# Kernel tuning notes

Hardware: AMD Instinct MI355X
Metric: run time of the kernel (lower is better)

The kernel has to match this reference:

```python
import jax, jax.numpy as jnp
import numpy as np

N_NODES = 50000
N_EDGES = 800000
N_FEAT = 128
N_GRAPHS = 512
OUT_DIM = 128


def gcn_conv(x, W, b, src, dst, ew, n):
    """PyG GCNConv: h = x @ W; add self-loops (weight 1); symmetric norm
    D^-1/2 A D^-1/2 with edge weights; scatter-add messages src->dst; + bias."""
    h = x @ W  # [n, out]
    loop = jnp.arange(n)
    s = jnp.concatenate([src, loop])
    d = jnp.concatenate([dst, loop])
    w = jnp.concatenate([ew, jnp.ones((n,), x.dtype)])
    deg = jax.ops.segment_sum(w, d, num_segments=n)
    dinv = jnp.where(deg > 0, jax.lax.rsqrt(deg), 0.0)
    norm = dinv[s] * w * dinv[d]  # [E+n]
    out = jax.ops.segment_sum(h[s] * norm[:, None], d, num_segments=n)
    return out + b


def setup_inputs() -> dict:
    key = jax.random.key(0)
    ks = jax.random.split(key, 12)
    F = N_FEAT
    x = jax.random.normal(ks[0], (N_NODES, F), jnp.float32)
    edge_index = jax.random.randint(ks[1], (2, N_EDGES), 0, N_NODES, jnp.int64)
    edge_attr = jax.random.uniform(ks[2], (N_EDGES,), jnp.float32)
    # deterministic sorted graph assignment -> no empty graphs (avoids -inf in max pool)
    batch = (jnp.arange(N_NODES, dtype=jnp.int64) * N_GRAPHS) // N_NODES
    def lin(k, fi, fo):
        s = 1.0 / np.sqrt(fi)
        return jax.random.uniform(k, (fi, fo), jnp.float32, -s, s)
    return {
        "x": x, "edge_attr": edge_attr,
        "W1": lin(ks[3], F, F), "b1": jnp.zeros((F,), jnp.float32),
        "W2": lin(ks[4], F, 2 * F), "b2": jnp.zeros((2 * F,), jnp.float32),
        "W3": lin(ks[5], 2 * F, 4 * F), "b3": jnp.zeros((4 * F,), jnp.float32),
        "Wf1": lin(ks[6], 4 * F, 1024), "bf1": jnp.zeros((1024,), jnp.float32),
        "Wf2": lin(ks[7], 1024, OUT_DIM), "bf2": jnp.zeros((OUT_DIM,), jnp.float32),
        "edge_index": edge_index, "batch": batch,
    }


def reference(x, edge_attr, W1, b1, W2, b2, W3, b3, Wf1, bf1, Wf2, bf2,
              edge_index, batch):
    n = x.shape[0]
    src, dst = edge_index[0], edge_index[1]
    h = jax.nn.relu(gcn_conv(x, W1, b1, src, dst, edge_attr, n))
    h = jax.nn.relu(gcn_conv(h, W2, b2, src, dst, edge_attr, n))
    h = jax.nn.relu(gcn_conv(h, W3, b3, src, dst, edge_attr, n))
    # global max pool over nodes per graph
    g = jax.ops.segment_max(h, batch, num_segments=N_GRAPHS)  # [G, 4F]
    g = jax.nn.relu(g @ Wf1 + bf1)
    # dropout is identity in eval mode
    out = g @ Wf2 + bf2
    return out
```

## Files before the change

kernel.cpp:

```cpp
#include <hip/hip_runtime.h>

#define NNODES 50000
#define NEDGES 800000
#define NGRAPH 512
#define DCAP 64

typedef short bf16x8 __attribute__((ext_vector_type(8)));
typedef unsigned short u16x8 __attribute__((ext_vector_type(8)));
typedef float f32x4 __attribute__((ext_vector_type(4)));
typedef unsigned long long u64;

static __device__ __forceinline__ float b2f(unsigned short u) {
    return __uint_as_float(((unsigned)u) << 16);
}
static __device__ __forceinline__ unsigned short f2b(float f) {
    unsigned u = __float_as_uint(f);
    unsigned r = (u + 0x7fffu + ((u >> 16) & 1u)) >> 16;
    return (unsigned short)r;
}

static __device__ __forceinline__ void ldrow(const unsigned short* X, size_t off, float (&v)[2]) {
    unsigned u = *(const unsigned*)(X + off);
    v[0] = b2f((unsigned short)(u & 0xffff));
    v[1] = b2f((unsigned short)(u >> 16));
}
static __device__ __forceinline__ void ldrow(const unsigned short* X, size_t off, float (&v)[4]) {
    uint2 u = *(const uint2*)(X + off);
    v[0] = b2f((unsigned short)(u.x & 0xffff));
    v[1] = b2f((unsigned short)(u.x >> 16));
    v[2] = b2f((unsigned short)(u.y & 0xffff));
    v[3] = b2f((unsigned short)(u.y >> 16));
}

__global__ void k_setup(u64* deg_cnt, int* gp) {
    int i = blockIdx.x * 256 + threadIdx.x;
    if (i < NNODES) deg_cnt[i] = (u64)(1u << 24);
    if (i < NGRAPH * 512) gp[i] = 0;
}

__global__ __launch_bounds__(256) void k_count(const int4* __restrict__ ei_s,
                                               const int4* __restrict__ ei_d,
                                               const float4* __restrict__ ew4,
                                               u64* deg_cnt,
                                               unsigned* __restrict__ edges) {
    int t = blockIdx.x * 256 + threadIdx.x;
    if (t >= NEDGES / 4) return;
    int4 ss = ei_s[t];
    int4 dd = ei_d[t];
    float4 ww = ew4[t];
    int s[4] = {ss.x, ss.y, ss.z, ss.w};
    int d[4] = {dd.x, dd.y, dd.z, dd.w};
    float w[4] = {ww.x, ww.y, ww.z, ww.w};
    int slot[4];
    #pragma unroll
    for (int u = 0; u < 4; ++u) {
        unsigned fixed = __float2uint_rn(w[u] * 16777216.0f);
        u64 old = atomicAdd(&deg_cnt[d[u]], ((u64)1 << 32) | fixed);
        slot[u] = (int)(old >> 32);
        if (slot[u] > DCAP - 1) slot[u] = DCAP - 1;
    }
    #pragma unroll
    for (int u = 0; u < 4; ++u)
        edges[((unsigned)d[u] << 6) | slot[u]] = ((unsigned)f2b(w[u]) << 16) | (unsigned)s[u];
}

__global__ void k_prep(const u64* __restrict__ deg_cnt, float* __restrict__ dinv) {
    int i = blockIdx.x * 256 + threadIdx.x;
    if (i < NNODES)
        dinv[i] = rsqrtf((float)(unsigned)(deg_cnt[i] & 0xffffffffull) * 5.9604645e-8f);
}

__global__ void k_wt_all(const float* __restrict__ W1, const float* __restrict__ W2,
                         const float* __restrict__ W3, const float* __restrict__ Wf1,
                         const float* __restrict__ Wf2,
                         unsigned short* __restrict__ T1, unsigned short* __restrict__ T2,
                         unsigned short* __restrict__ T3, unsigned short* __restrict__ Tf1,
                         unsigned short* __restrict__ Tf2) {
    int i = blockIdx.x * 256 + threadIdx.x;
    const float* W; unsigned short* T; int K, ns;
    if (i < 16384)        { W = W1;  T = T1;  K = 128;  ns = 7;  }
    else if (i < 49152)   { W = W2;  T = T2;  K = 128;  ns = 8;  i -= 16384; }
    else if (i < 180224)  { W = W3;  T = T3;  K = 256;  ns = 9;  i -= 49152; }
    else if (i < 704512)  { W = Wf1; T = Tf1; K = 512;  ns = 10; i -= 180224; }
    else if (i < 835584)  { W = Wf2; T = Tf2; K = 1024; ns = 7;  i -= 704512; }
    else return;
    int k = i >> ns, n = i & ((1 << ns) - 1);
    T[(size_t)n * K + k] = f2b(W[i]);
}

__global__ void k_cvt4(const float* __restrict__ X, const float* __restrict__ dinv,
                       unsigned short* __restrict__ Y, int n4) {
    int i = blockIdx.x * 256 + threadIdx.x;
    if (i < n4) {
        float4 v = ((const float4*)X)[i];
        float d = dinv[i >> 5];
        uint2 o;
        o.x = (unsigned)f2b(v.x * d) | ((unsigned)f2b(v.y * d) << 16);
        o.y = (unsigned)f2b(v.z * d) | ((unsigned)f2b(v.w * d) << 16);
        ((uint2*)Y)[i] = o;
    }
}

template <int VEC>
__global__ __launch_bounds__(256) void k_aggregate(const unsigned short* __restrict__ X,
                                                   const u64* __restrict__ deg_cnt,
                                                   const unsigned* __restrict__ edges,
                                                   const float* __restrict__ dinv,
                                                   unsigned short* __restrict__ Z) {
    const int F = 64 * VEC;
    const int wave = threadIdx.x >> 6, lane = threadIdx.x & 63;
    const int node = blockIdx.x * 4 + wave;
    if (node >= NNODES) return;
    const int fo = lane * VEC;
    const float di = dinv[node];
    const int cnt = (int)(deg_cnt[node] >> 32);
    const unsigned* erow = edges + ((unsigned)node << 6);

    float acc[VEC], v[VEC];
    ldrow(X, (size_t)node * F + fo, v);
    #pragma unroll
    for (int j = 0; j < VEC; ++j) acc[j] = v[j];

    int e = 0;
    for (; e + 8 <= cnt; e += 8) {
        unsigned pk[8];
        float vv[8][VEC];
        #pragma unroll
        for (int u = 0; u < 8; ++u) pk[u] = erow[e + u];
        #pragma unroll
        for (int u = 0; u < 8; ++u) ldrow(X, (size_t)(pk[u] & 0xffffu) * F + fo, vv[u]);
        #pragma unroll
        for (int u = 0; u < 8; ++u) {
            float c = b2f((unsigned short)(pk[u] >> 16));
            #pragma unroll
            for (int j = 0; j < VEC; ++j) acc[j] += c * vv[u][j];
        }
    }
    for (; e + 4 <= cnt; e += 4) {
        unsigned pk[4];
        float vv[4][VEC];
        #pragma unroll
        for (int u = 0; u < 4; ++u) pk[u] = erow[e + u];
        #pragma unroll
        for (int u = 0; u < 4; ++u) ldrow(X, (size_t)(pk[u] & 0xffffu) * F + fo, vv[u]);
        #pragma unroll
        for (int u = 0; u < 4; ++u) {
            float c = b2f((unsigned short)(pk[u] >> 16));
            #pragma unroll
            for (int j = 0; j < VEC; ++j) acc[j] += c * vv[u][j];
        }
    }
    for (; e < cnt; ++e) {
        unsigned pe = erow[e];
        float c = b2f((unsigned short)(pe >> 16));
        ldrow(X, (size_t)(pe & 0xffffu) * F + fo, v);
        #pragma unroll
        for (int j = 0; j < VEC; ++j) acc[j] += c * v[j];
    }

    if constexpr (VEC == 2) {
        unsigned o = (unsigned)f2b(di * acc[0]) | ((unsigned)f2b(di * acc[1]) << 16);
        *(unsigned*)(Z + (size_t)node * F + fo) = o;
    } else {
        uint2 o;
        o.x = (unsigned)f2b(di * acc[0]) | ((unsigned)f2b(di * acc[1]) << 16);
        o.y = (unsigned)f2b(di * acc[2]) | ((unsigned)f2b(di * acc[3]) << 16);
        *(uint2*)(Z + (size_t)node * F + fo) = o;
    }
}

template <int CMODE, int AFP>
__global__ __launch_bounds__(256) void k_gemm_mfma(const void* __restrict__ Av,
                                                   const unsigned short* __restrict__ WT,
                                                   const float* __restrict__ bias,
                                                   void* __restrict__ Cv,
                                                   const int* __restrict__ batch,
                                                   int* __restrict__ gp,
                                                   const float* __restrict__ rscale,
                                                   int M, int N, int K) {
    constexpr int LDK = 40;
    __shared__ unsigned short As[64 * LDK];
    __shared__ unsigned short Bs[128 * LDK];
    const int tid = threadIdx.x;
    const int m0 = blockIdx.y * 64, n0 = blockIdx.x * 128;
    const int wave = tid >> 6, lane = tid & 63;
    const int wm = (wave >> 1) * 32;
    const int wn = (wave & 1) * 64;
    const int quad = lane >> 4, mrow = lane & 15;

    const int ar = tid >> 2;
    const int ak = (tid & 3) * 8;
    const bool arow_ok = (m0 + ar) < M;
    const size_t aoff = (size_t)(m0 + ar) * K + ak;
    const unsigned short* Bg0 = WT + (size_t)(n0 + ar) * K + ak;
    const unsigned short* Bg1 = WT + (size_t)(n0 + ar + 64) * K + ak;

    f32x4 acc[2][4] = {};

    for (int k0 = 0; k0 < K; k0 += 32) {
        u16x8 av = {};
        if (arow_ok) {
            if constexpr (AFP) {
                const float* Af = (const float*)Av + aoff + k0;
                float4 f0 = *(const float4*)Af;
                float4 f1 = *(const float4*)(Af + 4);
                av[0] = (short)f2b(f0.x); av[1] = (short)f2b(f0.y);
                av[2] = (short)f2b(f0.z); av[3] = (short)f2b(f0.w);
                av[4] = (short)f2b(f1.x); av[5] = (short)f2b(f1.y);
                av[6] = (short)f2b(f1.z); av[7] = (short)f2b(f1.w);
            } else {
                av = *(const u16x8*)((const unsigned short*)Av + aoff + k0);
            }
        }
        u16x8 bv0 = *(const u16x8*)(Bg0 + k0);
        u16x8 bv1 = *(const u16x8*)(Bg1 + k0);
        *(u16x8*)&As[ar * LDK + ak] = av;
        *(u16x8*)&Bs[ar * LDK + ak] = bv0;
        *(u16x8*)&Bs[(ar + 64) * LDK + ak] = bv1;
        __syncthreads();
        bf16x8 af[2], bf[4];
        #pragma unroll
        for (int mt = 0; mt < 2; ++mt)
            af[mt] = *(const bf16x8*)&As[(wm + mt * 16 + mrow) * LDK + quad * 8];
        #pragma unroll
        for (int nt = 0; nt < 4; ++nt)
            bf[nt] = *(const bf16x8*)&Bs[(wn + nt * 16 + mrow) * LDK + quad * 8];
        #pragma unroll
        for (int mt = 0; mt < 2; ++mt)
            #pragma unroll
            for (int nt = 0; nt < 4; ++nt)
                acc[mt][nt] = __builtin_amdgcn_mfma_f32_16x16x32_bf16(af[mt], bf[nt], acc[mt][nt], 0, 0, 0);
        __syncthreads();
    }

    float bn[4];
    #pragma unroll
    for (int nt = 0; nt < 4; ++nt) bn[nt] = bias[n0 + wn + nt * 16 + mrow];

    if constexpr (CMODE == 0) {
        unsigned short* C = (unsigned short*)Cv;
        #pragma unroll
        for (int mt = 0; mt < 2; ++mt) {
            #pragma unroll
            for (int r = 0; r < 4; ++r) {
                int row = m0 + wm + mt * 16 + quad * 4 + r;
                if (row < M) {
                    float rs = rscale ? rscale[row] : 1.0f;
                    #pragma unroll
                    for (int nt = 0; nt < 4; ++nt) {
                        float v = fmaxf(acc[mt][nt][r] + bn[nt], 0.f) * rs;
                        C[(size_t)row * N + n0 + wn + nt * 16 + mrow] = f2b(v);
                    }
                }
            }
        }
    } else if constexpr (CMODE == 1) {
        float* C = (float*)Cv;
        #pragma unroll
        for (int mt = 0; mt < 2; ++mt) {
            #pragma unroll
            for (int r = 0; r < 4; ++r) {
                int row = m0 + wm + mt * 16 + quad * 4 + r;
                if (row < M) {
                    #pragma unroll
                    for (int nt = 0; nt < 4; ++nt)
                        C[(size_t)row * N + n0 + wn + nt * 16 + mrow] = acc[mt][nt][r] + bn[nt];
                }
            }
        }
    } else {
        __shared__ float pools[2][2][128];
        const int g0 = batch[m0];
        int last = m0 + 63; if (last >= M) last = M - 1;
        const int gl = batch[last];
        int  gid[8];
        bool rok[8];
        #pragma unroll
        for (int mt = 0; mt < 2; ++mt)
            #pragma unroll
            for (int r = 0; r < 4; ++r) {
                int row = m0 + wm + mt * 16 + quad * 4 + r;
                rok[mt * 4 + r] = row < M;
                gid[mt * 4 + r] = (row < M) ? batch[row] : -1;
            }
        #pragma unroll
        for (int nt = 0; nt < 4; ++nt) {
            float v0 = 0.f, v1 = 0.f;
            #pragma unroll
            for (int mt = 0; mt < 2; ++mt)
                #pragma unroll
                for (int r = 0; r < 4; ++r) {
                    if (rok[mt * 4 + r]) {
                        float v = fmaxf(acc[mt][nt][r] + bn[nt], 0.f);
                        if (gid[mt * 4 + r] == g0) v0 = fmaxf(v0, v);
                        else v1 = fmaxf(v1, v);
                    }
                }
            v0 = fmaxf(v0, __shfl_xor(v0, 16, 64));
            v0 = fmaxf(v0, __shfl_xor(v0, 32, 64));
            v1 = fmaxf(v1, __shfl_xor(v1, 16, 64));
            v1 = fmaxf(v1, __shfl_xor(v1, 32, 64));
            if (quad == 0) {
                int c = wn + nt * 16 + mrow;
                pools[wm >> 5][0][c] = v0;
                pools[wm >> 5][1][c] = v1;
            }
        }
        __syncthreads();
        int c = tid & 127, gi = tid >> 7;
        float v = fmaxf(pools[0][gi][c], pools[1][gi][c]);
        int g = gi ? gl : g0;
        if (gi == 0 || gl != g0)
            atomicMax(&gp[(size_t)g * N + n0 + c], __float_as_int(v));
    }
}

extern "C" void kernel_launch(void* const* d_in, const int* in_sizes, int n_in,
                              void* d_out, int out_size, void* d_ws, size_t ws_size,
                              hipStream_t stream) {
    const float* x   = (const float*)d_in[0];
    const float* ew  = (const float*)d_in[1];
    const float* W1  = (const float*)d_in[2];
    const float* b1  = (const float*)d_in[3];
    const float* W2  = (const float*)d_in[4];
    const float* b2  = (const float*)d_in[5];
    const float* W3  = (const float*)d_in[6];
    const float* b3  = (const float*)d_in[7];
    const float* Wf1 = (const float*)d_in[8];
    const float* bf1 = (const float*)d_in[9];
    const float* Wf2 = (const float*)d_in[10];
    const float* bf2 = (const float*)d_in[11];
    const int* ei    = (const int*)d_in[12];
    const int* batch = (const int*)d_in[13];
    float* out = (float*)d_out;
    (void)in_sizes; (void)n_in; (void)out_size; (void)ws_size;

    char* p = (char*)d_ws;
    auto alloc = [&](size_t bytes) -> char* {
        char* r = p;
        p += (bytes + 255) & ~(size_t)255;
        return r;
    };
    const int nbN = (NNODES + 255) / 256;
    u64*   deg_cnt = (u64*)alloc((size_t)NNODES * 8);
    float* dinv   = (float*)alloc((size_t)NNODES * 4);
    unsigned* edges = (unsigned*)alloc((size_t)NNODES * DCAP * 4);
    int*   gp     = (int*)  alloc((size_t)NGRAPH * 512 * 4);
    unsigned short* f1   = (unsigned short*)alloc((size_t)NGRAPH * 1024 * 2);
    unsigned short* wt1  = (unsigned short*)alloc((size_t)128 * 128 * 2);
    unsigned short* wt2  = (unsigned short*)alloc((size_t)256 * 128 * 2);
    unsigned short* wt3  = (unsigned short*)alloc((size_t)512 * 256 * 2);
    unsigned short* wtf1 = (unsigned short*)alloc((size_t)1024 * 512 * 2);
    unsigned short* wtf2 = (unsigned short*)alloc((size_t)128 * 1024 * 2);
    unsigned short* bufA = (unsigned short*)alloc((size_t)NNODES * 256 * 2);
    unsigned short* bufB = (unsigned short*)alloc((size_t)NNODES * 256 * 2);
    unsigned short* x16  = bufB;

    const int MB = (NNODES + 63) / 64;
    const int AGG = (NNODES + 3) / 4;

    k_setup<<<1024, 256, 0, stream>>>(deg_cnt, gp);
    k_count<<<(NEDGES / 4 + 255) / 256, 256, 0, stream>>>(
        (const int4*)ei, (const int4*)(ei + NEDGES), (const float4*)ew, deg_cnt, edges);
    k_prep<<<nbN, 256, 0, stream>>>(deg_cnt, dinv);
    k_wt_all<<<(835584 + 255) / 256, 256, 0, stream>>>(W1, W2, W3, Wf1, Wf2,
                                                       wt1, wt2, wt3, wtf1, wtf2);
    k_cvt4<<<(NNODES * 32 + 255) / 256, 256, 0, stream>>>(x, dinv, x16, NNODES * 32);

    k_aggregate<2><<<AGG, 256, 0, stream>>>(x16, deg_cnt, edges, dinv, bufA);
    k_gemm_mfma<0, 0><<<dim3(1, MB), 256, 0, stream>>>(bufA, wt1, b1, bufB, batch, nullptr, dinv, NNODES, 128, 128);
    k_aggregate<2><<<AGG, 256, 0, stream>>>(bufB, deg_cnt, edges, dinv, bufA);
    k_gemm_mfma<0, 0><<<dim3(2, MB), 256, 0, stream>>>(bufA, wt2, b2, bufB, batch, nullptr, dinv, NNODES, 256, 128);
    k_aggregate<4><<<AGG, 256, 0, stream>>>(bufB, deg_cnt, edges, dinv, bufA);
    k_gemm_mfma<2, 0><<<dim3(4, MB), 256, 0, stream>>>(bufA, wt3, b3, nullptr, batch, gp, nullptr, NNODES, 512, 256);

    k_gemm_mfma<0, 1><<<dim3(8, NGRAPH / 64), 256, 0, stream>>>(gp, wtf1, bf1, f1, batch, nullptr, nullptr, NGRAPH, 1024, 512);
    k_gemm_mfma<1, 0><<<dim3(1, NGRAPH / 64), 256, 0, stream>>>(f1, wtf2, bf2, out, batch, nullptr, nullptr, NGRAPH, 128, 1024);
}
```

Measured before the change: 374.1 us.

## Use 16-byte gathers with edge-parallel lane groups and software pipelining in aggregation

```diff
diff --git a/kernel.cpp b/kernel.cpp
--- a/kernel.cpp
+++ b/kernel.cpp
@@ -19,17 +19,13 @@
     return (unsigned short)r;
 }
 
-static __device__ __forceinline__ void ldrow(const unsigned short* X, size_t off, float (&v)[2]) {
-    unsigned u = *(const unsigned*)(X + off);
-    v[0] = b2f((unsigned short)(u & 0xffff));
-    v[1] = b2f((unsigned short)(u >> 16));
-}
-static __device__ __forceinline__ void ldrow(const unsigned short* X, size_t off, float (&v)[4]) {
-    uint2 u = *(const uint2*)(X + off);
-    v[0] = b2f((unsigned short)(u.x & 0xffff));
-    v[1] = b2f((unsigned short)(u.x >> 16));
-    v[2] = b2f((unsigned short)(u.y & 0xffff));
-    v[3] = b2f((unsigned short)(u.y >> 16));
+static __device__ __forceinline__ void accum8(float (&acc)[8], float c, uint4 v) {
+    unsigned w[4] = {v.x, v.y, v.z, v.w};
+    #pragma unroll
+    for (int i = 0; i < 4; ++i) {
+        acc[2 * i]     += c * __uint_as_float(w[i] << 16);
+        acc[2 * i + 1] += c * __uint_as_float(w[i] & 0xffff0000u);
+    }
 }
 
 __global__ void k_setup(u64* deg_cnt, int* gp) {
@@ -101,71 +97,84 @@
     }
 }
 
-template <int VEC>
+template <int F>
 __global__ __launch_bounds__(256) void k_aggregate(const unsigned short* __restrict__ X,
                                                    const u64* __restrict__ deg_cnt,
                                                    const unsigned* __restrict__ edges,
                                                    const float* __restrict__ dinv,
                                                    unsigned short* __restrict__ Z) {
-    const int F = 64 * VEC;
+    constexpr int LPR = F / 8;
+    constexpr int GRP = 64 / LPR;
+    constexpr int STEP = GRP * 2;
     const int wave = threadIdx.x >> 6, lane = threadIdx.x & 63;
     const int node = blockIdx.x * 4 + wave;
     if (node >= NNODES) return;
-    const int fo = lane * VEC;
+    const int sub = lane & (LPR - 1);
+    const int grp = lane / LPR;
+    const int fo = sub * 8;
+    const unsigned short* Xf = X + fo;
     const float di = dinv[node];
     const int cnt = (int)(deg_cnt[node] >> 32);
     const unsigned* erow = edges + ((unsigned)node << 6);
 
-    float acc[VEC], v[VEC];
-    ldrow(X, (size_t)node * F + fo, v);
-    #pragma unroll
-    for (int j = 0; j < VEC; ++j) acc[j] = v[j];
-
-    int e = 0;
-    for (; e + 8 <= cnt; e += 8) {
-        unsigned pk[8];
-        float vv[8][VEC];
-        #pragma unroll
-        for (int u = 0; u < 8; ++u) pk[u] = erow[e + u];
-        #pragma unroll
-        for (int u = 0; u < 8; ++u) ldrow(X, (size_t)(pk[u] & 0xffffu) * F + fo, vv[u]);
-        #pragma unroll
-        for (int u = 0; u < 8; ++u) {
-            float c = b2f((unsigned short)(pk[u] >> 16));
-            #pragma unroll
-            for (int j = 0; j < VEC; ++j) acc[j] += c * vv[u][j];
-        }
-    }
-    for (; e + 4 <= cnt; e += 4) {
-        unsigned pk[4];
-        float vv[4][VEC];
-        #pragma unroll
-        for (int u = 0; u < 4; ++u) pk[u] = erow[e + u];
-        #pragma unroll
-        for (int u = 0; u < 4; ++u) ldrow(X, (size_t)(pk[u] & 0xffffu) * F + fo, vv[u]);
-        #pragma unroll
-        for (int u = 0; u < 4; ++u) {
-            float c = b2f((unsigned short)(pk[u] >> 16));
-            #pragma unroll
-            for (int j = 0; j < VEC; ++j) acc[j] += c * vv[u][j];
-        }
-    }
-    for (; e < cnt; ++e) {
-        unsigned pe = erow[e];
-        float c = b2f((unsigned short)(pe >> 16));
-        ldrow(X, (size_t)(pe & 0xffffu) * F + fo, v);
-        #pragma unroll
-        for (int j = 0; j < VEC; ++j) acc[j] += c * v[j];
-    }
-
-    if constexpr (VEC == 2) {
-        unsigned o = (unsigned)f2b(di * acc[0]) | ((unsigned)f2b(di * acc[1]) << 16);
-        *(unsigned*)(Z + (size_t)node * F + fo) = o;
-    } else {
-        uint2 o;
-        o.x = (unsigned)f2b(di * acc[0]) | ((unsigned)f2b(di * acc[1]) << 16);
-        o.y = (unsigned)f2b(di * acc[2]) | ((unsigned)f2b(di * acc[3]) << 16);
-        *(uint2*)(Z + (size_t)node * F + fo) = o;
+    const uint4 selfv = *(const uint4*)(Xf + (size_t)node * F);
+
+    float acc[8] = {};
+
+    const int e0 = grp;
+    const int nb = (cnt + STEP - 1) / STEP;
+
+    unsigned pa0 = 0, pb0 = 0, pa1 = 0, pb1 = 0;
+    uint4 va0 = {}, vb0 = {};
+    if (nb > 0) {
+        int ea = e0, eb = e0 + GRP;
+        pa0 = (ea < cnt) ? erow[ea] : 0u;
+        pb0 = (eb < cnt) ? erow[eb] : 0u;
+        va0 = *(const uint4*)(Xf + (size_t)(pa0 & 0xffffu) * F);
+        vb0 = *(const uint4*)(Xf + (size_t)(pb0 & 0xffffu) * F);
+        if (nb > 1) {
+            int ea1 = e0 + STEP, eb1 = ea1 + GRP;
+            pa1 = (ea1 < cnt) ? erow[ea1] : 0u;
+            pb1 = (eb1 < cnt) ? erow[eb1] : 0u;
+        }
+    }
+    for (int p = 0; p < nb; ++p) {
+        uint4 va1 = {}, vb1 = {};
+        unsigned pa2 = 0, pb2 = 0;
+        if (p + 1 < nb) {
+            va1 = *(const uint4*)(Xf + (size_t)(pa1 & 0xffffu) * F);
+            vb1 = *(const uint4*)(Xf + (size_t)(pb1 & 0xffffu) * F);
+            if (p + 2 < nb) {
+                int ea = e0 + (p + 2) * STEP, eb = ea + GRP;
+                pa2 = (ea < cnt) ? erow[ea] : 0u;
+                pb2 = (eb < cnt) ? erow[eb] : 0u;
+            }
+        }
+        accum8(acc, b2f((unsigned short)(pa0 >> 16)), va0);
+        accum8(acc, b2f((unsigned short)(pb0 >> 16)), vb0);
+        pa0 = pa1; pb0 = pb1; va0 = va1; vb0 = vb1;
+        pa1 = pa2; pb1 = pb2;
+    }
+
+    #pragma unroll
+    for (int j = 0; j < 8; ++j) {
+        if constexpr (GRP == 4) acc[j] += __shfl_xor(acc[j], 16, 64);
+        acc[j] += __shfl_xor(acc[j], 32, 64);
+    }
+
+    if (grp == 0) {
+        unsigned w[4] = {selfv.x, selfv.y, selfv.z, selfv.w};
+        unsigned o[4];
+        #pragma unroll
+        for (int i = 0; i < 4; ++i) {
+            float s0 = __uint_as_float(w[i] << 16);
+            float s1 = __uint_as_float(w[i] & 0xffff0000u);
+            unsigned short c0 = f2b(di * (acc[2 * i] + s0));
+            unsigned short c1 = f2b(di * (acc[2 * i + 1] + s1));
+            o[i] = (unsigned)c0 | ((unsigned)c1 << 16);
+        }
+        uint4 ov; ov.x = o[0]; ov.y = o[1]; ov.z = o[2]; ov.w = o[3];
+        *(uint4*)(Z + (size_t)node * F + fo) = ov;
     }
 }
 
@@ -367,11 +376,11 @@
                                                        wt1, wt2, wt3, wtf1, wtf2);
     k_cvt4<<<(NNODES * 32 + 255) / 256, 256, 0, stream>>>(x, dinv, x16, NNODES * 32);
 
-    k_aggregate<2><<<AGG, 256, 0, stream>>>(x16, deg_cnt, edges, dinv, bufA);
+    k_aggregate<128><<<AGG, 256, 0, stream>>>(x16, deg_cnt, edges, dinv, bufA);
     k_gemm_mfma<0, 0><<<dim3(1, MB), 256, 0, stream>>>(bufA, wt1, b1, bufB, batch, nullptr, dinv, NNODES, 128, 128);
-    k_aggregate<2><<<AGG, 256, 0, stream>>>(bufB, deg_cnt, edges, dinv, bufA);
+    k_aggregate<128><<<AGG, 256, 0, stream>>>(bufB, deg_cnt, edges, dinv, bufA);
     k_gemm_mfma<0, 0><<<dim3(2, MB), 256, 0, stream>>>(bufA, wt2, b2, bufB, batch, nullptr, dinv, NNODES, 256, 128);
-    k_aggregate<4><<<AGG, 256, 0, stream>>>(bufB, deg_cnt, edges, dinv, bufA);
+    k_aggregate<256><<<AGG, 256, 0, stream>>>(bufB, deg_cnt, edges, dinv, bufA);
     k_gemm_mfma<2, 0><<<dim3(4, MB), 256, 0, stream>>>(bufA, wt3, b3, nullptr, batch, gp, nullptr, NNODES, 512, 256);
 
     k_gemm_mfma<0, 1><<<dim3(8, NGRAPH / 64), 256, 0, stream>>>(gp, wtf1, bf1, f1, batch, nullptr, nullptr, NGRAPH, 1024, 512);
```

Result: no change. 371.1 us (-0.8%).
